# Kernel tuning notes

Measured on AMD Instinct MI355X. Metric: run time of the kernel, lower is better.

Reference implementation:

```python
import jax, jax.numpy as jnp
import numpy as np

NUM_NODES = 50000
D_IN, D_HID, D_OUT = 128, 128, 40
NUM_EDGES = 800000


def setup_inputs() -> dict:
    key = jax.random.key(0)
    ks = jax.random.split(key, 10)
    x = jax.random.normal(ks[0], (NUM_NODES, D_IN), dtype=jnp.float32)
    edge_index = jax.random.randint(ks[1], (2, NUM_EDGES), 0, NUM_NODES, dtype=jnp.int64)
    # GCNConv weights (lin: in -> out), glorot-style init; bias init zeros per bias_init
    def glorot(k, fan_in, fan_out):
        lim = np.sqrt(6.0 / (fan_in + fan_out)).astype(np.float32)
        return jax.random.uniform(k, (fan_in, fan_out), jnp.float32, -lim, lim)
    W0 = glorot(ks[2], D_IN, D_HID)
    b0 = jnp.zeros((D_HID,), jnp.float32)
    W1 = glorot(ks[3], D_HID, D_HID)
    b1 = jnp.zeros((D_HID,), jnp.float32)
    W2 = glorot(ks[4], D_HID, D_OUT)
    b2 = jnp.zeros((D_OUT,), jnp.float32)
    return {"x": x, "edge_index": edge_index,
            "W0": W0, "b0": b0, "W1": W1, "b1": b1, "W2": W2, "b2": b2}


def _gcn_conv(h, src, dst, W, b):
    # linear projection then gather from source nodes, scatter-add to dest nodes
    hW = h @ W                                   # [N, out]
    msg = jnp.take(hW, src, axis=0)              # [E, out]
    agg = jax.ops.segment_sum(msg, dst, num_segments=NUM_NODES)  # [N, out]
    return agg + b


def reference(x, edge_index, W0, b0, W1, b1, W2, b2):
    src, dst = edge_index[0], edge_index[1]
    h = jax.nn.relu(_gcn_conv(x, src, dst, W0, b0))
    h = jax.nn.relu(_gcn_conv(h, src, dst, W1, b1))
    return _gcn_conv(h, src, dst, W2, b2)
```

## Files before the change

### kernel.cpp

```cpp
#include <hip/hip_runtime.h>

#define NN 50000
#define EE 800000

#define BKT 196
#define GB  334
#define EPB 2396
#define CAPB 6144
#define CAP 5120
#define ECAP 1536
#define ECAP6 512

typedef unsigned char u8;
typedef unsigned short u16;
typedef unsigned int u32;
typedef __attribute__((ext_vector_type(8))) short short8;
typedef __attribute__((ext_vector_type(4))) float f32x4;
typedef __attribute__((ext_vector_type(2))) float f32x2;
typedef __attribute__((ext_vector_type(4))) unsigned int u32x4;
typedef __attribute__((ext_vector_type(4))) unsigned short ushort4v;

__device__ __forceinline__ float b2f(u16 u) {
    return __uint_as_float(((unsigned)u) << 16);
}
__device__ __forceinline__ u16 f2b(float f) {
    unsigned u = __float_as_uint(f);
    return (u16)((u + 0x7FFF + ((u >> 16) & 1)) >> 16);
}

#if defined(__has_builtin)
#if __has_builtin(__builtin_amdgcn_cvt_pk_f32_fp8) && __has_builtin(__builtin_amdgcn_cvt_pk_fp8_f32)
#define HW_FP8 1
#endif
#endif

#ifdef HW_FP8
__device__ __forceinline__ void dec4(u32 w, float* f) {
    f32x2 lo = __builtin_amdgcn_cvt_pk_f32_fp8(w, false);
    f32x2 hi = __builtin_amdgcn_cvt_pk_f32_fp8(w, true);
    f[0] = lo[0]; f[1] = lo[1]; f[2] = hi[0]; f[3] = hi[1];
}
__device__ __forceinline__ u8 enc1(float v) {
    return (u8)(__builtin_amdgcn_cvt_pk_fp8_f32(v, v, 0, false) & 0xFF);
}
#else
__device__ __forceinline__ float dec1(u8 b) {
    u32 m = b & 0x7F;
    if (m < 8) return 0.f;
    u32 u = ((u32)(b & 0x80) << 24) | ((m + (120u << 3)) << 20);
    return __uint_as_float(u);
}
__device__ __forceinline__ void dec4(u32 w, float* f) {
    f[0] = dec1((u8)(w & 0xFF));
    f[1] = dec1((u8)((w >> 8) & 0xFF));
    f[2] = dec1((u8)((w >> 16) & 0xFF));
    f[3] = dec1((u8)((w >> 24) & 0xFF));
}
__device__ __forceinline__ u8 enc1(float v) {
    u32 u = __float_as_uint(v);
    u32 mag = u & 0x7FFFFFFF;
    if (mag < 0x3C800000u) return 0;
    if (mag > 0x43E00000u) mag = 0x43E00000u;
    u32 r = mag + 0x7FFFFu + ((mag >> 20) & 1);
    u32 e = (r >> 20) - (120u << 3);
    if (e > 0x7E) e = 0x7E;
    return (u8)(((u >> 24) & 0x80) | e);
}
#endif

__device__ __forceinline__ void dec16(u32x4 v, float* f) {
    dec4(v.x, f);
    dec4(v.y, f + 4);
    dec4(v.z, f + 8);
    dec4(v.w, f + 12);
}

__global__ __launch_bounds__(256) void prep_init(
    const float* __restrict__ W0, const float* __restrict__ W1,
    const float* __restrict__ W2, u16* __restrict__ Wf,
    int* __restrict__ gCur)
{
    const int g = blockIdx.x, t = threadIdx.x;
    if (g == 24) {
        if (t < BKT) gCur[t] = t * CAPB;
        return;
    }
    int u = g * 4 + (t >> 6);
    int set = u >> 5, nt2 = (u >> 2) & 7, kt = u & 3;
    int lane = t & 63;
    const float* W = (set == 0) ? W0 : (set == 1) ? W1 : W2;
    int ld = (set == 2) ? 40 : 128;
    int ncols = (set == 2) ? 40 : 128;
    int n = nt2 * 16 + (lane & 15);
    int kb = kt * 32 + (lane >> 4) * 8;
    u16* dw = Wf + set * 16384 + (size_t)((nt2 * 4 + kt) * 64 + lane) * 8;
#pragma unroll
    for (int j = 0; j < 8; j++) {
        float v = (n < ncols) ? W[(kb + j) * ld + n] : 0.f;
        dw[j] = f2b(v);
    }
}

__global__ __launch_bounds__(256) void scatter_gemm0(
    const int* __restrict__ src, const int* __restrict__ dst,
    int* __restrict__ gCur, u32* __restrict__ pairs,
    const float* __restrict__ A, const u16* __restrict__ Wf,
    u8* __restrict__ out, int N, int E)
{
    __shared__ int cnt[BKT];
    __shared__ int cur[BKT];
    const int t = threadIdx.x;
    if (blockIdx.x < GB) {
        const int g = blockIdx.x;
        for (int b = t; b < BKT; b += 256) cnt[b] = 0;
        __syncthreads();
        const int beg = g * EPB, end = min(E, beg + EPB);
        for (int e = beg + t; e < end; e += 256)
            atomicAdd(&cnt[dst[e] >> 8], 1);
        __syncthreads();
        for (int b = t; b < BKT; b += 256)
            cur[b] = atomicAdd(&gCur[b], cnt[b]);
        __syncthreads();
        for (int e = beg + t; e < end; e += 256) {
            int d = dst[e];
            int pos = atomicAdd(&cur[d >> 8], 1);
            pairs[pos] = ((u32)src[e] << 8) | (u32)(d & 255);
        }
        return;
    }
    const int bx = blockIdx.x - GB;
    const int wave = t >> 6;
    const int lane = t & 63;
    const int m = lane & 15;
    const int q = lane >> 4;
    const int rowBase = bx * 64 + wave * 16;
    const int arow = rowBase + m;
    const bool rowOk = (arow < N);

    short8 af[4];
#pragma unroll
    for (int kt = 0; kt < 4; kt++) {
        if (rowOk) {
            float4 lo = *(const float4*)(A + (size_t)arow * 128 + kt * 32 + q * 8);
            float4 hi = *(const float4*)(A + (size_t)arow * 128 + kt * 32 + q * 8 + 4);
            short8 v;
            v[0] = (short)f2b(lo.x); v[1] = (short)f2b(lo.y);
            v[2] = (short)f2b(lo.z); v[3] = (short)f2b(lo.w);
            v[4] = (short)f2b(hi.x); v[5] = (short)f2b(hi.y);
            v[6] = (short)f2b(hi.z); v[7] = (short)f2b(hi.w);
            af[kt] = v;
        } else {
            af[kt] = (short8)0;
        }
    }

    f32x4 acc[8];
#pragma unroll
    for (int nt = 0; nt < 8; nt++) acc[nt] = (f32x4)0.f;

#pragma unroll
    for (int kt = 0; kt < 4; kt++) {
#pragma unroll
        for (int nt = 0; nt < 8; nt++) {
            short8 bf = *(const short8*)(Wf + (size_t)((nt * 4 + kt) * 64 + lane) * 8);
            acc[nt] = __builtin_amdgcn_mfma_f32_16x16x32_bf16(af[kt], bf, acc[nt], 0, 0, 0);
        }
    }

#pragma unroll
    for (int nt = 0; nt < 8; nt++) {
#pragma unroll
        for (int r = 0; r < 4; r++) {
            int orow = rowBase + q * 4 + r;
            if (orow < N) out[(size_t)orow * 128 + nt * 16 + m] = enc1(acc[nt][r]);
        }
    }
}

__global__ __launch_bounds__(256) void bucket_sort(
    const u32* __restrict__ pairs, const int* __restrict__ gCur,
    int* __restrict__ off, int* __restrict__ csr, int N, int E)
{
    __shared__ int sdeg[256];
    __shared__ int sex[256];
    __shared__ int scur[256];
    __shared__ int stage[CAP];
    const int b = blockIdx.x, t = threadIdx.x;

    int c0 = (t < BKT) ? (gCur[t] - t * CAPB) : 0;
    sex[t] = c0;
    __syncthreads();
    for (int d = 1; d < 256; d <<= 1) {
        int u = (t >= d) ? sex[t - d] : 0;
        __syncthreads();
        sex[t] += u;
        __syncthreads();
    }
    __shared__ int sBase, sCnt;
    if (t == b) { sBase = sex[t] - c0; sCnt = c0; }
    __syncthreads();
    const int base = sBase;
    const int cnt = sCnt;
    const int pbase = b * CAPB;
    __syncthreads();

    sdeg[t] = 0;
    __syncthreads();
    for (int i = t; i < cnt; i += 256)
        atomicAdd(&sdeg[pairs[pbase + i] & 255], 1);
    __syncthreads();

    int v = sdeg[t];
    sex[t] = v;
    __syncthreads();
    for (int d = 1; d < 256; d <<= 1) {
        int u = (t >= d) ? sex[t - d] : 0;
        __syncthreads();
        sex[t] += u;
        __syncthreads();
    }
    const int excl = sex[t] - v;
    const int node = b * 256 + t;
    if (node < N) off[node] = base + excl;
    if (b == BKT - 1 && t == 0) off[N] = E;
    scur[t] = excl;
    __syncthreads();

    if (cnt <= CAP) {
        for (int i = t; i < cnt; i += 256) {
            u32 p = pairs[pbase + i];
            int pos = atomicAdd(&scur[p & 255], 1);
            stage[pos] = (int)(p >> 8);
        }
        __syncthreads();
        for (int i = t; i < cnt; i += 256) csr[base + i] = stage[i];
    } else {
        for (int i = t; i < cnt; i += 256) {
            u32 p = pairs[pbase + i];
            int pos = atomicAdd(&scur[p & 255], 1);
            csr[base + pos] = (int)(p >> 8);
        }
    }
}

template<int NT, int OSTRIDE, int OCOLS, bool OFP8>
__global__ __launch_bounds__(512) void agg_gemm_t(
    const u8* __restrict__ val, const int* __restrict__ off,
    const int* __restrict__ csr, const float* __restrict__ bias,
    const u16* __restrict__ Wf, void* __restrict__ outp, int N)
{
    __shared__ u16 A[64][136];
    __shared__ int sIdx[ECAP];
    const int tid = threadIdx.x;
    const int rowBase = blockIdx.x * 64;

    const int rowEndN = min(rowBase + 64, N);
    const int blkBeg = off[rowBase];
    const int blkEnd = off[rowEndN];
    const int blkCnt = blkEnd - blkBeg;
    const bool useLds = (blkCnt <= ECAP);
    if (useLds) {
        for (int i = tid; i < blkCnt; i += 512) sIdx[i] = csr[blkBeg + i];
    }
    __syncthreads();
    const int ib = useLds ? blkBeg : 0;
    const int* ip = useLds ? (const int*)sIdx : csr;

    {
        const int c8 = tid & 7;
        const int nl = tid >> 3;
        const u8* vb = val + c8 * 16;
        const int node = rowBase + nl;
        const bool ok = (node < N);
        const int beg = (ok ? off[node] : 0) - ib;
        const int end = (ok ? off[node + 1] : 0) - ib;

        float a0[16], a1[16];
#pragma unroll
        for (int j = 0; j < 16; j++) { a0[j] = 0.f; a1[j] = 0.f; }

        int i = beg;
        for (; i + 3 < end; i += 4) {
            int s0 = ip[i], s1 = ip[i + 1], s2 = ip[i + 2], s3 = ip[i + 3];
            u32x4 v0 = *(const u32x4*)(vb + (size_t)s0 * 128);
            u32x4 v1 = *(const u32x4*)(vb + (size_t)s1 * 128);
            u32x4 v2 = *(const u32x4*)(vb + (size_t)s2 * 128);
            u32x4 v3 = *(const u32x4*)(vb + (size_t)s3 * 128);
            float f0[16], f1[16], f2[16], f3[16];
            dec16(v0, f0); dec16(v1, f1); dec16(v2, f2); dec16(v3, f3);
#pragma unroll
            for (int j = 0; j < 16; j++) {
                a0[j] += f0[j] + f2[j];
                a1[j] += f1[j] + f3[j];
            }
        }
        for (; i < end; i++) {
            int s0 = ip[i];
            u32x4 v0 = *(const u32x4*)(vb + (size_t)s0 * 128);
            float f0[16];
            dec16(v0, f0);
#pragma unroll
            for (int j = 0; j < 16; j++) a0[j] += f0[j];
        }

        float4 bA = *(const float4*)(bias + c8 * 16);
        float4 bB = *(const float4*)(bias + c8 * 16 + 4);
        float4 bC = *(const float4*)(bias + c8 * 16 + 8);
        float4 bD = *(const float4*)(bias + c8 * 16 + 12);
        float bb[16] = {bA.x, bA.y, bA.z, bA.w, bB.x, bB.y, bB.z, bB.w,
                        bC.x, bC.y, bC.z, bC.w, bD.x, bD.y, bD.z, bD.w};
        short8 o0, o1;
#pragma unroll
        for (int j = 0; j < 8; j++)
            o0[j] = (short)f2b(fmaxf(a0[j] + a1[j] + bb[j], 0.f));
#pragma unroll
        for (int j = 0; j < 8; j++)
            o1[j] = (short)f2b(fmaxf(a0[j + 8] + a1[j + 8] + bb[j + 8], 0.f));
        *(short8*)&A[nl][c8 * 16] = o0;
        *(short8*)&A[nl][c8 * 16 + 8] = o1;
    }
    __syncthreads();

    const int wave = tid >> 6;
    const int lane = tid & 63;
    const int m = lane & 15;
    const int q = lane >> 4;
    const int rg = wave & 3;
    const int ch = wave >> 2;
    const int lrow = rg * 16 + m;

    short8 af[4];
#pragma unroll
    for (int kt = 0; kt < 4; kt++)
        af[kt] = *(const short8*)&A[lrow][kt * 32 + q * 8];

    constexpr int NTH = (NT + 1) / 2;
    const int ntB = ch ? NTH : 0;
    const int ntE = ch ? NT : NTH;

    f32x4 acc[NTH];
#pragma unroll
    for (int i = 0; i < NTH; i++) acc[i] = (f32x4)0.f;

#pragma unroll
    for (int kt = 0; kt < 4; kt++) {
        for (int nt = ntB; nt < ntE; nt++) {
            short8 bf = *(const short8*)(Wf + (size_t)((nt * 4 + kt) * 64 + lane) * 8);
            acc[nt - ntB] = __builtin_amdgcn_mfma_f32_16x16x32_bf16(af[kt], bf, acc[nt - ntB], 0, 0, 0);
        }
    }

    for (int nt = ntB; nt < ntE; nt++) {
        const int col = nt * 16 + m;
        if (col < OCOLS) {
#pragma unroll
            for (int r = 0; r < 4; r++) {
                int orow = rowBase + rg * 16 + q * 4 + r;
                if (orow < N) {
                    if constexpr (OFP8) {
                        ((u8*)outp)[(size_t)orow * OSTRIDE + col] = enc1(acc[nt - ntB][r]);
                    } else {
                        ((u16*)outp)[(size_t)orow * OSTRIDE + col] = f2b(acc[nt - ntB][r]);
                    }
                }
            }
        }
    }
}

__global__ __launch_bounds__(256) void agg40b(
    const u16* __restrict__ val, const int* __restrict__ off,
    const int* __restrict__ csr, const float* __restrict__ b2,
    float* __restrict__ out, int N)
{
    __shared__ int sIdx[ECAP6];
    const int t = threadIdx.x;
    const int nodeBase = blockIdx.x * 16;
    const int nodeEndN = min(nodeBase + 16, N);
    const int blkBeg = off[nodeBase];
    const int blkEnd = off[nodeEndN];
    const int blkCnt = blkEnd - blkBeg;
    const bool useLds = (blkCnt <= ECAP6);
    if (useLds) {
        for (int i = t; i < blkCnt; i += 256) sIdx[i] = csr[blkBeg + i];
    }
    __syncthreads();
    const int ib = useLds ? blkBeg : 0;
    const int* ip = useLds ? (const int*)sIdx : csr;

    const int c = t & 15;
    const int node = nodeBase + (t >> 4);
    if (node >= N || c >= 10) return;
    const int beg = off[node] - ib, end = off[node + 1] - ib;

    float a0[4] = {0, 0, 0, 0};
    float a1[4] = {0, 0, 0, 0};
    int i = beg;
    for (; i + 1 < end; i += 2) {
        int s0 = ip[i];
        int s1 = ip[i + 1];
        ushort4v v0 = *(const ushort4v*)(val + (size_t)s0 * 40 + c * 4);
        ushort4v v1 = *(const ushort4v*)(val + (size_t)s1 * 40 + c * 4);
        a0[0] += b2f(v0.x); a0[1] += b2f(v0.y); a0[2] += b2f(v0.z); a0[3] += b2f(v0.w);
        a1[0] += b2f(v1.x); a1[1] += b2f(v1.y); a1[2] += b2f(v1.z); a1[3] += b2f(v1.w);
    }
    if (i < end) {
        int s0 = ip[i];
        ushort4v v0 = *(const ushort4v*)(val + (size_t)s0 * 40 + c * 4);
        a0[0] += b2f(v0.x); a0[1] += b2f(v0.y); a0[2] += b2f(v0.z); a0[3] += b2f(v0.w);
    }
    float4 b = *(const float4*)(b2 + c * 4);
    float4 r;
    r.x = a0[0] + a1[0] + b.x;
    r.y = a0[1] + a1[1] + b.y;
    r.z = a0[2] + a1[2] + b.z;
    r.w = a0[3] + a1[3] + b.w;
    *(float4*)(out + (size_t)node * 40 + c * 4) = r;
}

extern "C" void kernel_launch(void* const* d_in, const int* in_sizes, int n_in,
                              void* d_out, int out_size, void* d_ws, size_t ws_size,
                              hipStream_t stream)
{
    const float* x  = (const float*)d_in[0];
    const int*   ei = (const int*)d_in[1];
    const float* W0 = (const float*)d_in[2];
    const float* b0 = (const float*)d_in[3];
    const float* W1 = (const float*)d_in[4];
    const float* b1 = (const float*)d_in[5];
    const float* W2 = (const float*)d_in[6];
    const float* b2 = (const float*)d_in[7];
    float* out = (float*)d_out;

    const int N = NN, E = EE;
    const int* src = ei;
    const int* dst = ei + E;

    char* ws = (char*)d_ws;
    u8*  t     = (u8*)ws;
    u8*  tB    = (u8*)(ws + 6400000);
    u16* t2    = (u16*)(ws + 12800000);
    u16* Wf    = (u16*)(ws + 16800000);
    int* off   = (int*)(ws + 16900000);
    int* csr   = (int*)(ws + 17100008);
    int* gCur  = (int*)(ws + 20300008);
    u32* pairs = (u32*)(ws + 20300800);

    const int tileGrid = (N + 63) / 64;
    const int agg40Grid = (N + 15) / 16;

    prep_init<<<25, 256, 0, stream>>>(W0, W1, W2, Wf, gCur);
    scatter_gemm0<<<GB + tileGrid, 256, 0, stream>>>(src, dst, gCur, pairs,
                                                     x, Wf, t, N, E);
    bucket_sort<<<BKT, 256, 0, stream>>>(pairs, gCur, off, csr, N, E);

    agg_gemm_t<8, 128, 128, true><<<tileGrid, 512, 0, stream>>>(
        t, off, csr, b0, Wf + 16384, (void*)tB, N);
    agg_gemm_t<3, 40, 40, false><<<tileGrid, 512, 0, stream>>>(
        tB, off, csr, b1, Wf + 32768, (void*)t2, N);
    agg40b<<<agg40Grid, 256, 0, stream>>>(t2, off, csr, b2, out, N);
}
```

Baseline: 191.9 us.

## Split each node's edge list across two thread groups and halve agg tile rows

The fused aggregate+GEMM kernel now handles 32 rows per block instead of 64. Each node's neighbour list is split between two 8-thread groups, and the partial sums are combined through a shared-memory buffer before bias, ReLU and bf16 packing. The MFMA stage is re-split into 2 row groups by 4 column groups, and launch bounds now request higher occupancy. The aim is to double the parallelism in the gather loop, hiding memory latency and balancing uneven node degrees. The cost is an extra barrier, extra LDS, more blocks, and NT=3 leaving some waves idle in the GEMM.

```diff
diff --git a/kernel.cpp b/kernel.cpp
--- a/kernel.cpp
+++ b/kernel.cpp
@@ -8,7 +8,7 @@
 #define EPB 2396
 #define CAPB 6144
 #define CAP 5120
-#define ECAP 1536
+#define ECAP 1024
 #define ECAP6 512
 
 typedef unsigned char u8;
@@ -244,17 +244,18 @@
 }
 
 template<int NT, int OSTRIDE, int OCOLS, bool OFP8>
-__global__ __launch_bounds__(512) void agg_gemm_t(
+__global__ __launch_bounds__(512, 8) void agg_gemm_t(
     const u8* __restrict__ val, const int* __restrict__ off,
     const int* __restrict__ csr, const float* __restrict__ bias,
     const u16* __restrict__ Wf, void* __restrict__ outp, int N)
 {
-    __shared__ u16 A[64][136];
+    __shared__ u16 A[32][136];
+    __shared__ float P[32][128];
     __shared__ int sIdx[ECAP];
     const int tid = threadIdx.x;
-    const int rowBase = blockIdx.x * 64;
-
-    const int rowEndN = min(rowBase + 64, N);
+    const int rowBase = blockIdx.x * 32;
+
+    const int rowEndN = min(rowBase + 32, N);
     const int blkBeg = off[rowBase];
     const int blkEnd = off[rowEndN];
     const int blkCnt = blkEnd - blkBeg;
@@ -268,16 +269,21 @@
 
     {
         const int c8 = tid & 7;
-        const int nl = tid >> 3;
+        const int h = (tid >> 3) & 1;
+        const int nl = tid >> 4;
         const u8* vb = val + c8 * 16;
         const int node = rowBase + nl;
         const bool ok = (node < N);
-        const int beg = (ok ? off[node] : 0) - ib;
-        const int end = (ok ? off[node + 1] : 0) - ib;
-
-        float a0[16], a1[16];
-#pragma unroll
-        for (int j = 0; j < 16; j++) { a0[j] = 0.f; a1[j] = 0.f; }
+        const int fbeg = (ok ? off[node] : 0) - ib;
+        const int fend = (ok ? off[node + 1] : 0) - ib;
+        const int len = fend - fbeg;
+        const int mid = fbeg + ((len + 1) >> 1);
+        const int beg = h ? mid : fbeg;
+        const int end = h ? fend : mid;
+
+        float a[16];
+#pragma unroll
+        for (int j = 0; j < 16; j++) a[j] = 0.f;
 
         int i = beg;
         for (; i + 3 < end; i += 4) {
@@ -289,10 +295,8 @@
             float f0[16], f1[16], f2[16], f3[16];
             dec16(v0, f0); dec16(v1, f1); dec16(v2, f2); dec16(v3, f3);
 #pragma unroll
-            for (int j = 0; j < 16; j++) {
-                a0[j] += f0[j] + f2[j];
-                a1[j] += f1[j] + f3[j];
-            }
+            for (int j = 0; j < 16; j++)
+                a[j] += (f0[j] + f1[j]) + (f2[j] + f3[j]);
         }
         for (; i < end; i++) {
             int s0 = ip[i];
@@ -300,24 +304,31 @@
             float f0[16];
             dec16(v0, f0);
 #pragma unroll
-            for (int j = 0; j < 16; j++) a0[j] += f0[j];
-        }
-
-        float4 bA = *(const float4*)(bias + c8 * 16);
-        float4 bB = *(const float4*)(bias + c8 * 16 + 4);
-        float4 bC = *(const float4*)(bias + c8 * 16 + 8);
-        float4 bD = *(const float4*)(bias + c8 * 16 + 12);
-        float bb[16] = {bA.x, bA.y, bA.z, bA.w, bB.x, bB.y, bB.z, bB.w,
-                        bC.x, bC.y, bC.z, bC.w, bD.x, bD.y, bD.z, bD.w};
-        short8 o0, o1;
-#pragma unroll
-        for (int j = 0; j < 8; j++)
-            o0[j] = (short)f2b(fmaxf(a0[j] + a1[j] + bb[j], 0.f));
-#pragma unroll
-        for (int j = 0; j < 8; j++)
-            o1[j] = (short)f2b(fmaxf(a0[j + 8] + a1[j + 8] + bb[j + 8], 0.f));
-        *(short8*)&A[nl][c8 * 16] = o0;
-        *(short8*)&A[nl][c8 * 16 + 8] = o1;
+            for (int j = 0; j < 16; j++) a[j] += f0[j];
+        }
+
+        if (h) {
+#pragma unroll
+            for (int j = 0; j < 16; j++) P[nl][c8 * 16 + j] = a[j];
+        }
+        __syncthreads();
+        if (!h) {
+            float4 bA = *(const float4*)(bias + c8 * 16);
+            float4 bB = *(const float4*)(bias + c8 * 16 + 4);
+            float4 bC = *(const float4*)(bias + c8 * 16 + 8);
+            float4 bD = *(const float4*)(bias + c8 * 16 + 12);
+            float bb[16] = {bA.x, bA.y, bA.z, bA.w, bB.x, bB.y, bB.z, bB.w,
+                            bC.x, bC.y, bC.z, bC.w, bD.x, bD.y, bD.z, bD.w};
+            short8 o0, o1;
+#pragma unroll
+            for (int j = 0; j < 8; j++)
+                o0[j] = (short)f2b(fmaxf(a[j] + P[nl][c8 * 16 + j] + bb[j], 0.f));
+#pragma unroll
+            for (int j = 0; j < 8; j++)
+                o1[j] = (short)f2b(fmaxf(a[j + 8] + P[nl][c8 * 16 + 8 + j] + bb[j + 8], 0.f));
+            *(short8*)&A[nl][c8 * 16] = o0;
+            *(short8*)&A[nl][c8 * 16 + 8] = o1;
+        }
     }
     __syncthreads();
 
@@ -325,8 +336,8 @@
     const int lane = tid & 63;
     const int m = lane & 15;
     const int q = lane >> 4;
-    const int rg = wave & 3;
-    const int ch = wave >> 2;
+    const int rg = wave & 1;
+    const int cg = wave >> 1;
     const int lrow = rg * 16 + m;
 
     short8 af[4];
@@ -334,13 +345,13 @@
     for (int kt = 0; kt < 4; kt++)
         af[kt] = *(const short8*)&A[lrow][kt * 32 + q * 8];
 
-    constexpr int NTH = (NT + 1) / 2;
-    const int ntB = ch ? NTH : 0;
-    const int ntE = ch ? NT : NTH;
-
-    f32x4 acc[NTH];
-#pragma unroll
-    for (int i = 0; i < NTH; i++) acc[i] = (f32x4)0.f;
+    constexpr int NTW = (NT + 3) / 4;
+    const int ntB = cg * NTW;
+    const int ntE = min(ntB + NTW, NT);
+
+    f32x4 acc[NTW];
+#pragma unroll
+    for (int i = 0; i < NTW; i++) acc[i] = (f32x4)0.f;
 
 #pragma unroll
     for (int kt = 0; kt < 4; kt++) {
@@ -446,17 +457,18 @@
     int* gCur  = (int*)(ws + 20300008);
     u32* pairs = (u32*)(ws + 20300800);
 
-    const int tileGrid = (N + 63) / 64;
+    const int g0Grid = GB + (N + 63) / 64;
+    const int aggGrid = (N + 31) / 32;
     const int agg40Grid = (N + 15) / 16;
 
     prep_init<<<25, 256, 0, stream>>>(W0, W1, W2, Wf, gCur);
-    scatter_gemm0<<<GB + tileGrid, 256, 0, stream>>>(src, dst, gCur, pairs,
-                                                     x, Wf, t, N, E);
+    scatter_gemm0<<<g0Grid, 256, 0, stream>>>(src, dst, gCur, pairs,
+                                              x, Wf, t, N, E);
     bucket_sort<<<BKT, 256, 0, stream>>>(pairs, gCur, off, csr, N, E);
 
-    agg_gemm_t<8, 128, 128, true><<<tileGrid, 512, 0, stream>>>(
+    agg_gemm_t<8, 128, 128, true><<<aggGrid, 512, 0, stream>>>(
         t, off, csr, b0, Wf + 16384, (void*)tB, N);
-    agg_gemm_t<3, 40, 40, false><<<tileGrid, 512, 0, stream>>>(
+    agg_gemm_t<3, 40, 40, false><<<aggGrid, 512, 0, stream>>>(
         tB, off, csr, b1, Wf + 32768, (void*)t2, N);
     agg40b<<<agg40Grid, 256, 0, stream>>>(t2, off, csr, b2, out, N);
 }
```

Result: slower. 283.7 us (+47.8%).
